# Kernel tuning notes

Measured on AMD Instinct MI355X. Metric: run time of the kernel, lower is better.

## Reference

```python
import jax, jax.numpy as jnp
import numpy as np

NUM_HEADS = 12
DIM = 768
NV = 4  # number of views
EPS = 1e-6


def _ln(x, g, b):
    m = x.mean(-1, keepdims=True)
    v = ((x - m) ** 2).mean(-1, keepdims=True)
    return (x - m) / jnp.sqrt(v + EPS) * g + b


def setup_inputs() -> dict:
    key = jax.random.key(0)
    ks = jax.random.split(key, 10)
    B, N, C, H = 4, 256, DIM, NUM_HEADS
    Hid = 4 * C
    s = 0.02
    return {
        'X': jax.random.normal(ks[0], (B * NV, N, C), jnp.float32),
        'norm1_g': jnp.ones((C,), jnp.float32),
        'norm1_b': jnp.zeros((C,), jnp.float32),
        'qkv_w': jax.random.normal(ks[1], (NV, 3 * C, C), jnp.float32) * s,
        'proj_w': jax.random.normal(ks[2], (NV, C, C), jnp.float32) * s,
        'proj_b': jnp.zeros((NV, C), jnp.float32),
        'norm2_g': jnp.ones((NV, C), jnp.float32),
        'norm2_b': jnp.zeros((NV, C), jnp.float32),
        'fc1_w': jax.random.normal(ks[3], (NV, Hid, C), jnp.float32) * s,
        'fc1_b': jnp.zeros((NV, Hid), jnp.float32),
        'fc2_w': jax.random.normal(ks[4], (NV, C, Hid), jnp.float32) * s,
        'fc2_b': jnp.zeros((NV, C), jnp.float32),
        'query': jax.random.normal(ks[5], (1, 1, C), jnp.float32),
        'mha_in_w': jax.random.normal(ks[6], (NV, 3 * C, C), jnp.float32) * s,
        'mha_in_b': jnp.zeros((NV, 3 * C), jnp.float32),
        'mha_out_w': jax.random.normal(ks[7], (NV, C, C), jnp.float32) * s,
        'mha_out_b': jnp.zeros((NV, C), jnp.float32),
    }


def reference(X, norm1_g, norm1_b, qkv_w, proj_w, proj_b, norm2_g, norm2_b,
              fc1_w, fc1_b, fc2_w, fc2_b, query, mha_in_w, mha_in_b,
              mha_out_w, mha_out_b):
    B4, N, C = X.shape
    B = B4 // NV
    H = NUM_HEADS
    hd = C // H
    scale = hd ** -0.5

    Xv = X.reshape(B, NV, N, C)
    Xn = _ln(Xv, norm1_g, norm1_b)

    # ---- FusionAttention: 4x4 pairwise cross attention between views ----
    qkv = jnp.einsum('bvnc,vdc->vbnd', Xn, qkv_w)              # [V,B,N,3C]
    qkv = qkv.reshape(NV, B, N, 3, H, hd).transpose(3, 0, 1, 4, 2, 5)  # [3,V,B,H,N,hd]
    q, k, v = qkv[0], qkv[1], qkv[2]
    scores = jnp.einsum('ibhnd,jbhmd->ijbhnm', q, k) * scale   # [V,V,B,H,N,N]
    attn = jax.nn.softmax(scores, axis=-1)
    ctx = jnp.einsum('ijbhnm,jbhmd->ijbhnd', attn, v)
    ctx = ctx.transpose(0, 1, 2, 4, 3, 5).reshape(NV, NV, B, N, C)
    # proj_i is affine, so mean over j of proj(x_j) == proj(mean_j x_j)
    ctx_mean = ctx.mean(axis=1)                                # [V,B,N,C]
    xa = jnp.einsum('vbnc,voc->vbno', ctx_mean, proj_w) + proj_b[:, None, None, :]

    x = xa * 2.0
    h = _ln(x, norm2_g[:, None, None, :], norm2_b[:, None, None, :])
    h1 = jax.nn.gelu(jnp.einsum('vbnc,vhc->vbnh', h, fc1_w) + fc1_b[:, None, None, :],
                     approximate=False)
    h2 = jnp.einsum('vbnh,vch->vbnc', h1, fc2_w) + fc2_b[:, None, None, :]
    x = x + h2                                                  # [V,B,N,C]

    # ---- CrossAttentionWithLearnableQuery (query identical for all T,B) ----
    wq, wk, wv = jnp.split(mha_in_w, 3, axis=1)                 # each [V,C,C]
    bq, bk, bv = jnp.split(mha_in_b, 3, axis=1)                 # each [V,C]
    q0 = query.reshape(C)
    qh = (jnp.einsum('c,vdc->vd', q0, wq) + bq).reshape(NV, H, hd)
    kh = (jnp.einsum('vbnc,vdc->vbnd', x, wk) + bk[:, None, None, :]).reshape(NV, B, N, H, hd)
    vh = (jnp.einsum('vbnc,vdc->vbnd', x, wv) + bv[:, None, None, :]).reshape(NV, B, N, H, hd)
    s2 = jnp.einsum('vhd,vbnhd->vbhn', qh, kh) * scale
    a2 = jax.nn.softmax(s2, axis=-1)
    c2 = jnp.einsum('vbhn,vbnhd->vbhd', a2, vh).reshape(NV, B, C)
    o = jnp.einsum('vbc,voc->vbo', c2, mha_out_w) + mha_out_b[:, None, :]  # [V,B,C]
    o = o.transpose(1, 0, 2).reshape(B, NV * C)                 # concat views
    # every query position produces identical output -> broadcast over T=N
    return jnp.broadcast_to(o[:, None, :], (B, N, NV * C))
```

## Files before the change

kernel.cpp:

```cpp
#include <hip/hip_runtime.h>
#include <math.h>

#define NVIEW 4
#define BATCH 4
#define NSEQ  256
#define CDIM  768
#define HEADS 12
#define HD    64

typedef __attribute__((ext_vector_type(8))) short   short8;
typedef __attribute__((ext_vector_type(8))) unsigned short ushort8;
typedef __attribute__((ext_vector_type(4))) float   float4v;

typedef const __attribute__((address_space(1))) void gas_t;
typedef       __attribute__((address_space(3))) void las_t;

__device__ __forceinline__ unsigned short f2b(float x)
{
    union { float f; unsigned u; } c; c.f = x;
    unsigned r = (c.u + 0x7FFFu + ((c.u >> 16) & 1u)) >> 16;
    return (unsigned short)r;
}

__global__ void conv_bf16(const float* __restrict__ src, unsigned short* __restrict__ dst, int n)
{
    int idx = (blockIdx.x * 256 + threadIdx.x) * 8;
    if (idx >= n) return;
    float4 a = *(const float4*)(src + idx);
    float4 b = *(const float4*)(src + idx + 4);
    ushort8 o;
    o[0] = f2b(a.x); o[1] = f2b(a.y); o[2] = f2b(a.z); o[3] = f2b(a.w);
    o[4] = f2b(b.x); o[5] = f2b(b.y); o[6] = f2b(b.z); o[7] = f2b(b.w);
    *(ushort8*)(dst + idx) = o;
}

__device__ __forceinline__ void block_ln_row_b(const float* __restrict__ xrow,
                                               const float* __restrict__ g,
                                               const float* __restrict__ b,
                                               unsigned short* __restrict__ orow)
{
    const int t = threadIdx.x;
    float x0 = xrow[t], x1 = xrow[t + 256], x2 = xrow[t + 512];
    float s  = x0 + x1 + x2;
    float s2 = x0 * x0 + x1 * x1 + x2 * x2;
    #pragma unroll
    for (int off = 32; off > 0; off >>= 1) {
        s  += __shfl_down(s, off);
        s2 += __shfl_down(s2, off);
    }
    __shared__ float w1[4], w2[4];
    if ((t & 63) == 0) { w1[t >> 6] = s; w2[t >> 6] = s2; }
    __syncthreads();
    float S  = w1[0] + w1[1] + w1[2] + w1[3];
    float S2 = w2[0] + w2[1] + w2[2] + w2[3];
    float mean = S * (1.0f / 768.0f);
    float var  = S2 * (1.0f / 768.0f) - mean * mean;
    float inv  = rsqrtf(var + 1e-6f);
    orow[t]       = f2b((x0 - mean) * inv * g[t]       + b[t]);
    orow[t + 256] = f2b((x1 - mean) * inv * g[t + 256] + b[t + 256]);
    orow[t + 512] = f2b((x2 - mean) * inv * g[t + 512] + b[t + 512]);
}

__global__ void ln1_kernel(const float* __restrict__ X, const float* __restrict__ g,
                           const float* __restrict__ b, unsigned short* __restrict__ Xn)
{
    int rid = blockIdx.x;
    int n  = rid & 255;
    int bv = rid >> 8;
    int bb = bv >> 2, v = bv & 3;
    const float* xrow = X + (long)rid * CDIM;
    unsigned short* orow = Xn + ((long)(v * 4 + bb) * 256 + n) * CDIM;
    block_ln_row_b(xrow, g, b, orow);
}

__global__ void ln2_kernel(const float* __restrict__ Xin, const float* __restrict__ g,
                           const float* __restrict__ b, unsigned short* __restrict__ Out)
{
    int rid = blockIdx.x;
    int v = rid >> 10;
    const float* xrow = Xin + (long)rid * CDIM;
    block_ln_row_b(xrow, g + v * CDIM, b + v * CDIM, Out + (long)rid * CDIM);
}

template <int EPI, int TM, typename OT>
__launch_bounds__(256, 2)
__global__ void gemm_bf16(const unsigned short* __restrict__ A,
                          const unsigned short* __restrict__ W,
                          const float* __restrict__ bias, const float* __restrict__ resid,
                          OT* __restrict__ out, int M, int N, int K,
                          long wStride, long wOff, int bStride, int bOff)
{
    const int v = blockIdx.z;
    const unsigned short* Av = A + (long)v * M * K;
    const unsigned short* Wv = W + v * wStride + wOff;

    __shared__ unsigned short As[TM * 64];
    __shared__ unsigned short Bs[128 * 64];

    const int tid  = threadIdx.x;
    const int lane = tid & 63;
    const int wave = tid >> 6;
    const int l15  = lane & 15;
    const int quad = lane >> 4;
    const int row0 = blockIdx.y * TM, col0 = blockIdx.x * 128;

    constexpr int MI = 4;
    constexpr int NI = (TM == 128) ? 4 : 2;
    const int mw = (TM == 128) ? (wave & 1) * 64 : 0;
    const int nw = (TM == 128) ? (wave >> 1) * 64 : wave * 32;

    float4v acc[MI][NI];
    #pragma unroll
    for (int i = 0; i < MI; ++i)
        #pragma unroll
        for (int j = 0; j < NI; ++j)
            acc[i][j] = (float4v){0.f, 0.f, 0.f, 0.f};

    const int lr8 = lane >> 3;
    const int p8  = lane & 7;

    for (int k0 = 0; k0 < K; k0 += 64) {
        __syncthreads();
        #pragma unroll
        for (int g = 0; g < TM / 32; ++g) {
            int G = wave * (TM / 32) + g;
            int r = G * 8 + lr8;
            int c = p8 ^ (r & 7);
            const unsigned short* sa = Av + (long)(row0 + r) * K + k0 + c * 8;
            __builtin_amdgcn_global_load_lds((gas_t*)sa, (las_t*)&As[G * 512], 16, 0, 0);
        }
        #pragma unroll
        for (int g = 0; g < 4; ++g) {
            int G = wave * 4 + g;
            int r = G * 8 + lr8;
            int c = p8 ^ (r & 7);
            const unsigned short* sw = Wv + (long)(col0 + r) * K + k0 + c * 8;
            __builtin_amdgcn_global_load_lds((gas_t*)sw, (las_t*)&Bs[G * 512], 16, 0, 0);
        }
        __syncthreads();

        #pragma unroll
        for (int ks = 0; ks < 2; ++ks) {
            short8 af[MI], bfr[NI];
            #pragma unroll
            for (int mi = 0; mi < MI; ++mi) {
                int m = mw + mi * 16 + l15;
                int p = (ks * 4 + quad) ^ (m & 7);
                af[mi] = *(const short8*)&As[m * 64 + p * 8];
            }
            #pragma unroll
            for (int ni = 0; ni < NI; ++ni) {
                int n = nw + ni * 16 + l15;
                int p = (ks * 4 + quad) ^ (n & 7);
                bfr[ni] = *(const short8*)&Bs[n * 64 + p * 8];
            }
            #pragma unroll
            for (int mi = 0; mi < MI; ++mi)
                #pragma unroll
                for (int ni = 0; ni < NI; ++ni)
                    acc[mi][ni] = __builtin_amdgcn_mfma_f32_16x16x32_bf16(af[mi], bfr[ni], acc[mi][ni], 0, 0, 0);
        }
    }

    #pragma unroll
    for (int mi = 0; mi < MI; ++mi) {
        #pragma unroll
        for (int ni = 0; ni < NI; ++ni) {
            int rowb = row0 + mw + mi * 16 + quad * 4;
            int col  = col0 + nw + ni * 16 + l15;
            float bval = 0.f;
            if (EPI >= 1) bval = bias[v * bStride + bOff + col];
            #pragma unroll
            for (int r = 0; r < 4; ++r) {
                float x = acc[mi][ni][r] + bval;
                long off = (long)v * M * N + (long)(rowb + r) * N + col;
                if constexpr (EPI == 2) {
                    x = 0.5f * x * (1.0f + erff(x * 0.70710678118654752f));
                } else if constexpr (EPI == 3) {
                    x += resid[off];
                } else if constexpr (EPI == 4) {
                    x *= 2.0f;
                }
                if constexpr (sizeof(OT) == 2) ((unsigned short*)out)[off] = f2b(x);
                else                           ((float*)out)[off] = x;
            }
        }
    }
}

__launch_bounds__(256, 2)
__global__ void fusion_attn_mfma(const unsigned short* __restrict__ QKV,
                                 unsigned short* __restrict__ ctx)
{
    const int qt = blockIdx.x;
    const int b  = blockIdx.y / HEADS;
    const int h  = blockIdx.y % HEADS;
    const int i  = blockIdx.z;
    const int tid  = threadIdx.x;
    const int lane = tid & 63;
    const int wave = tid >> 6;
    const int l15  = lane & 15;
    const int quad = lane >> 4;

    __shared__ unsigned short Qs[64 * 72];
    __shared__ unsigned short Ks[128 * 64];
    __shared__ unsigned short Ps[64 * 136];
    __shared__ unsigned short Vt[64 * 136];

    {
        int r = tid >> 2, p16 = (tid & 3) * 16;
        const unsigned short* src = QKV + ((long)((i * 4 + b) * 256 + qt * 64 + r)) * 2304 + h * 64 + p16;
        *(ushort8*)(&Qs[r * 72 + p16])     = *(const ushort8*)(src);
        *(ushort8*)(&Qs[r * 72 + p16 + 8]) = *(const ushort8*)(src + 8);
    }

    float4v acc_o[4];
    #pragma unroll
    for (int e = 0; e < 4; ++e) acc_o[e] = (float4v){0.f, 0.f, 0.f, 0.f};

    for (int j = 0; j < 4; ++j) {
        const unsigned short* Kb = QKV + ((long)((j * 4 + b) * 256)) * 2304 + 768 + h * 64;
        const unsigned short* Vb = Kb + 768;

        float4v sacc[16];
        #pragma unroll
        for (int t = 0; t < 16; ++t) sacc[t] = (float4v){0.f, 0.f, 0.f, 0.f};

        for (int half = 0; half < 2; ++half) {
            __syncthreads();
            #pragma unroll
            for (int g = 0; g < 4; ++g) {
                int R = wave * 32 + g * 8;
                int r = R + (lane >> 3);
                int p = lane & 7;
                int c = (p - (r & 7)) & 7;
                const unsigned short* src = Kb + (long)(half * 128 + r) * 2304 + c * 8;
                __builtin_amdgcn_global_load_lds((gas_t*)src, (las_t*)&Ks[R * 64], 16, 0, 0);
            }
            __syncthreads();
            #pragma unroll
            for (int ks = 0; ks < 2; ++ks) {
                int lcq = ks * 4 + quad;
                short8 qf = *(const short8*)&Qs[(wave * 16 + l15) * 72 + lcq * 8];
                #pragma unroll
                for (int nn = 0; nn < 8; ++nn) {
                    int n = nn * 16 + l15;
                    int p = (lcq + (n & 7)) & 7;
                    short8 kf = *(const short8*)&Ks[n * 64 + p * 8];
                    sacc[half * 8 + nn] =
                        __builtin_amdgcn_mfma_f32_16x16x32_bf16(qf, kf, sacc[half * 8 + nn], 0, 0, 0);
                }
            }
        }

        float rmax[4] = {-1e30f, -1e30f, -1e30f, -1e30f};
        #pragma unroll
        for (int t = 0; t < 16; ++t)
            #pragma unroll
            for (int r = 0; r < 4; ++r)
                rmax[r] = fmaxf(rmax[r], sacc[t][r] * 0.125f);
        #pragma unroll
        for (int off = 1; off < 16; off <<= 1)
            #pragma unroll
            for (int r = 0; r < 4; ++r)
                rmax[r] = fmaxf(rmax[r], __shfl_xor(rmax[r], off));
        float rsum[4] = {0.f, 0.f, 0.f, 0.f};
        #pragma unroll
        for (int t = 0; t < 16; ++t)
            #pragma unroll
            for (int r = 0; r < 4; ++r) {
                float e = __expf(sacc[t][r] * 0.125f - rmax[r]);
                sacc[t][r] = e;
                rsum[r] += e;
            }
        #pragma unroll
        for (int off = 1; off < 16; off <<= 1)
            #pragma unroll
            for (int r = 0; r < 4; ++r)
                rsum[r] += __shfl_xor(rsum[r], off);
        float invl[4];
        #pragma unroll
        for (int r = 0; r < 4; ++r) invl[r] = 1.0f / rsum[r];

        float4v pv[4];
        #pragma unroll
        for (int e = 0; e < 4; ++e) pv[e] = (float4v){0.f, 0.f, 0.f, 0.f};

        for (int half = 0; half < 2; ++half) {
            __syncthreads();
            #pragma unroll
            for (int nn = 0; nn < 8; ++nn)
                #pragma unroll
                for (int r = 0; r < 4; ++r)
                    Ps[(wave * 16 + quad * 4 + r) * 136 + nn * 16 + l15] = f2b(sacc[half * 8 + nn][r]);
            {
                int n = tid & 127;
                int c0 = (tid >> 7) * 4;
                #pragma unroll
                for (int cc = 0; cc < 4; ++cc) {
                    int c = c0 + cc;
                    ushort8 vv = *(const ushort8*)(Vb + (long)(half * 128 + n) * 2304 + c * 8);
                    #pragma unroll
                    for (int jj = 0; jj < 8; ++jj)
                        Vt[(c * 8 + jj) * 136 + n] = vv[jj];
                }
            }
            __syncthreads();
            #pragma unroll
            for (int ks = 0; ks < 4; ++ks) {
                int lc = ks * 4 + quad;
                short8 pf = *(const short8*)&Ps[(wave * 16 + l15) * 136 + lc * 8];
                #pragma unroll
                for (int et = 0; et < 4; ++et) {
                    short8 vf = *(const short8*)&Vt[(et * 16 + l15) * 136 + lc * 8];
                    pv[et] = __builtin_amdgcn_mfma_f32_16x16x32_bf16(pf, vf, pv[et], 0, 0, 0);
                }
            }
        }
        #pragma unroll
        for (int et = 0; et < 4; ++et)
            #pragma unroll
            for (int r = 0; r < 4; ++r)
                acc_o[et][r] += pv[et][r] * invl[r];
    }

    #pragma unroll
    for (int et = 0; et < 4; ++et)
        #pragma unroll
        for (int r = 0; r < 4; ++r) {
            int row = (i * 4 + b) * 256 + qt * 64 + wave * 16 + quad * 4 + r;
            int col = h * 64 + et * 16 + l15;
            ctx[(long)row * 768 + col] = f2b(acc_o[et][r] * 0.25f);
        }
}

__launch_bounds__(256, 4)
__global__ void qh_kernel(const float* __restrict__ query, const float* __restrict__ Win,
                          const float* __restrict__ Bin, float* __restrict__ QH)
{
    const int bi   = blockIdx.x;
    const int v    = bi / 192;
    const int dblk = bi - v * 192;
    const int t    = threadIdx.x;
    const int wave = t >> 6;
    const int lane = t & 63;
    const int d    = dblk * 4 + wave;

    __shared__ float qs[768];
    for (int idx = t; idx < 768; idx += 256) qs[idx] = query[idx];
    __syncthreads();

    const float* w = Win + ((long)v * 2304 + d) * 768;
    float acc = 0.f;
    #pragma unroll
    for (int k = 0; k < 3; ++k) {
        int c = k * 256 + lane * 4;
        float4 w4 = *(const float4*)(w + c);
        float4 q4 = *(const float4*)&qs[c];
        acc += w4.x * q4.x + w4.y * q4.y + w4.z * q4.z + w4.w * q4.w;
    }
    #pragma unroll
    for (int off = 32; off > 0; off >>= 1) acc += __shfl_down(acc, off);
    if (lane == 0)
        QH[v * 768 + d] = acc + Bin[(long)v * 2304 + d];
}

__launch_bounds__(256, 2)
__global__ void cross_attn(const float* __restrict__ KVH, const float* __restrict__ QH,
                           float* __restrict__ C2)
{
    const int h = blockIdx.x, b = blockIdx.y, v = blockIdx.z;
    const int t = threadIdx.x;
    __shared__ float qv[64];
    __shared__ float p[256];
    __shared__ float part[4][64];
    __shared__ float wred[4], wred2[4];

    if (t < 64) qv[t] = QH[(v * 12 + h) * 64 + t];
    __syncthreads();

    const float* krow = KVH + ((long)((v * 4 + b) * 256 + t)) * 1536 + h * 64;
    float s = 0.f;
    #pragma unroll
    for (int e = 0; e < 64; e += 4) {
        float4 k4 = *(const float4*)(krow + e);
        s += qv[e] * k4.x + qv[e + 1] * k4.y + qv[e + 2] * k4.z + qv[e + 3] * k4.w;
    }
    s *= 0.125f;
    float m4 = s;
    #pragma unroll
    for (int off = 32; off > 0; off >>= 1) m4 = fmaxf(m4, __shfl_down(m4, off));
    if ((t & 63) == 0) wred[t >> 6] = m4;
    __syncthreads();
    float rmax = fmaxf(fmaxf(wred[0], wred[1]), fmaxf(wred[2], wred[3]));
    float ev = __expf(s - rmax);
    p[t] = ev;
    float s4 = ev;
    #pragma unroll
    for (int off = 32; off > 0; off >>= 1) s4 += __shfl_down(s4, off);
    if ((t & 63) == 0) wred2[t >> 6] = s4;
    __syncthreads();
    float inv = 1.0f / (wred2[0] + wred2[1] + wred2[2] + wred2[3]);

    const int e = t & 63, ch = t >> 6;
    const float* vbase = KVH + ((long)((v * 4 + b) * 256)) * 1536 + 768 + h * 64 + e;
    float accv = 0.f;
    for (int m = ch * 64; m < ch * 64 + 64; ++m)
        accv += p[m] * vbase[(long)m * 1536];
    part[ch][e] = accv;
    __syncthreads();
    if (t < 64)
        C2[(v * 4 + b) * 768 + h * 64 + t] =
            (part[0][t] + part[1][t] + part[2][t] + part[3][t]) * inv;
}

__launch_bounds__(256, 4)
__global__ void out_matvec(const float* __restrict__ C2, const float* __restrict__ Wout,
                           const float* __restrict__ Bout, float* __restrict__ obc)
{
    const int bi   = blockIdx.x;
    const int v    = bi / 192;
    const int dblk = bi - v * 192;
    const int t    = threadIdx.x;
    const int wave = t >> 6;
    const int lane = t & 63;
    const int d    = dblk * 4 + wave;

    __shared__ float c2s[3072];
    #pragma unroll
    for (int idx = 0; idx < 3072; idx += 256) c2s[idx + t] = C2[v * 3072 + idx + t];
    __syncthreads();

    const float* w = Wout + ((long)v * 768 + d) * 768;
    float acc0 = 0.f, acc1 = 0.f, acc2 = 0.f, acc3 = 0.f;
    #pragma unroll
    for (int k = 0; k < 3; ++k) {
        int c = k * 256 + lane * 4;
        float4 w4 = *(const float4*)(w + c);
        float4 a0 = *(const float4*)&c2s[c];
        float4 a1 = *(const float4*)&c2s[768 + c];
        float4 a2 = *(const float4*)&c2s[1536 + c];
        float4 a3 = *(const float4*)&c2s[2304 + c];
        acc0 += w4.x * a0.x + w4.y * a0.y + w4.z * a0.z + w4.w * a0.w;
        acc1 += w4.x * a1.x + w4.y * a1.y + w4.z * a1.z + w4.w * a1.w;
        acc2 += w4.x * a2.x + w4.y * a2.y + w4.z * a2.z + w4.w * a2.w;
        acc3 += w4.x * a3.x + w4.y * a3.y + w4.z * a3.z + w4.w * a3.w;
    }
    #pragma unroll
    for (int off = 32; off > 0; off >>= 1) {
        acc0 += __shfl_down(acc0, off);
        acc1 += __shfl_down(acc1, off);
        acc2 += __shfl_down(acc2, off);
        acc3 += __shfl_down(acc3, off);
    }
    if (lane == 0) {
        float bb = Bout[v * 768 + d];
        obc[0 * 3072 + v * 768 + d] = acc0 + bb;
        obc[1 * 3072 + v * 768 + d] = acc1 + bb;
        obc[2 * 3072 + v * 768 + d] = acc2 + bb;
        obc[3 * 3072 + v * 768 + d] = acc3 + bb;
    }
}

__launch_bounds__(256, 4)
__global__ void out_bcast(const float* __restrict__ obc, float* __restrict__ out)
{
    const int b  = blockIdx.x >> 6;
    const int n0 = (blockIdx.x & 63) * 4;
    const int t  = threadIdx.x;
    const float4* src = (const float4*)(obc + (long)b * 3072);
    float4 v0 = src[t], v1 = src[t + 256], v2 = src[t + 512];
    float4* dst = (float4*)(out + ((long)(b * 256 + n0)) * 3072);
    #pragma unroll
    for (int r = 0; r < 4; ++r) {
        dst[r * 768 + t]       = v0;
        dst[r * 768 + t + 256] = v1;
        dst[r * 768 + t + 512] = v2;
    }
}

extern "C" void kernel_launch(void* const* d_in, const int* in_sizes, int n_in,
                              void* d_out, int out_size, void* d_ws, size_t ws_size,
                              hipStream_t stream)
{
    const float* X        = (const float*)d_in[0];
    const float* n1g      = (const float*)d_in[1];
    const float* n1b      = (const float*)d_in[2];
    const float* qkv_w    = (const float*)d_in[3];
    const float* proj_w   = (const float*)d_in[4];
    const float* proj_b   = (const float*)d_in[5];
    const float* n2g      = (const float*)d_in[6];
    const float* n2b      = (const float*)d_in[7];
    const float* fc1_w    = (const float*)d_in[8];
    const float* fc1_b    = (const float*)d_in[9];
    const float* fc2_w    = (const float*)d_in[10];
    const float* fc2_b    = (const float*)d_in[11];
    const float* query    = (const float*)d_in[12];
    const float* mha_in_w = (const float*)d_in[13];
    const float* mha_in_b = (const float*)d_in[14];
    const float* mha_out_w= (const float*)d_in[15];
    const float* mha_out_b= (const float*)d_in[16];
    float* out = (float*)d_out;

    char* wsb = (char*)d_ws;
    unsigned short* wbuf = (unsigned short*)wsb;
    unsigned short* rgA  = (unsigned short*)(wsb + 18874368);
    char*           rgB  = wsb + 25165824;
    float*          xbuf = (float*)(wsb + 50331648);
    float*          qh   = (float*)(wsb + 62914560);
    float*          c2   = (float*)(wsb + 62926848);
    float*          obc  = (float*)(wsb + 62976000);

    unsigned short* QKV = (unsigned short*)rgB;
    unsigned short* H1  = (unsigned short*)rgB;
    float*          KVH = (float*)rgB;

    conv_bf16<<<3456, 256, 0, stream>>>(qkv_w, wbuf, 7077888);
    ln1_kernel<<<4096, 256, 0, stream>>>(X, n1g, n1b, rgA);
    gemm_bf16<0, 128, unsigned short><<<dim3(18, 8, 4), 256, 0, stream>>>(
        rgA, wbuf, nullptr, nullptr, QKV, 1024, 2304, 768, 2304L * 768, 0, 0, 0);
    fusion_attn_mfma<<<dim3(4, 48, 4), 256, 0, stream>>>(QKV, rgA);
    conv_bf16<<<1152, 256, 0, stream>>>(proj_w, wbuf, 2359296);
    gemm_bf16<4, 64, float><<<dim3(6, 16, 4), 256, 0, stream>>>(
        rgA, wbuf, proj_b, nullptr, xbuf, 1024, 768, 768, 768L * 768, 0, 768, 0);
    ln2_kernel<<<4096, 256, 0, stream>>>(xbuf, n2g, n2b, rgA);
    conv_bf16<<<4608, 256, 0, stream>>>(fc1_w, wbuf, 9437184);
    gemm_bf16<2, 128, unsigned short><<<dim3(24, 8, 4), 256, 0, stream>>>(
        rgA, wbuf, fc1_b, nullptr, H1, 1024, 3072, 768, 3072L * 768, 0, 3072, 0);
    conv_bf16<<<4608, 256, 0, stream>>>(fc2_w, wbuf, 9437184);
    gemm_bf16<3, 64, unsigned short><<<dim3(6, 16, 4), 256, 0, stream>>>(
        H1, wbuf, fc2_b, xbuf, rgA, 1024, 768, 3072, 768L * 3072, 0, 768, 0);
    conv_bf16<<<3456, 256, 0, stream>>>(mha_in_w, wbuf, 7077888);
    gemm_bf16<1, 64, float><<<dim3(12, 16, 4), 256, 0, stream>>>(
        rgA, wbuf, mha_in_b, nullptr, KVH, 1024, 1536, 768, 2304L * 768, 768L * 768, 2304, 768);
    qh_kernel<<<768, 256, 0, stream>>>(query, mha_in_w, mha_in_b, qh);
    cross_attn<<<dim3(12, 4, 4), 256, 0, stream>>>(KVH, qh, c2);
    out_matvec<<<768, 256, 0, stream>>>(c2, mha_out_w, mha_out_b, obc);
    out_bcast<<<256, 256, 0, stream>>>(obc, out);
}
```

Baseline: 436.2 us.

## Restructure fusion attention: transposed MFMA, shared K/V buffer, prefetched V, packed stores

Rewrites the fusion attention kernel so the QK and PV MFMAs use swapped operands, which puts each query row in one lane and reduces the softmax to two cross-lane shuffles. K and the transposed V now share one LDS buffer, shrinking LDS so occupancy can rise to 3 blocks per CU. V loads are issued into registers ahead of time so they overlap with the QK MFMAs, with explicit waitcnt, barriers and setprio. P, V-transpose and output writes become packed 64-bit stores. The hand-placed waitcnt and barriers are more fragile, and the extra register pressure may clash with the higher occupancy bound.

Measured after the change: 425.0 us. 1.03x faster.

```diff
diff --git a/kernel.cpp b/kernel.cpp
--- a/kernel.cpp
+++ b/kernel.cpp
@@ -20,6 +20,11 @@
     union { float f; unsigned u; } c; c.f = x;
     unsigned r = (c.u + 0x7FFFu + ((c.u >> 16) & 1u)) >> 16;
     return (unsigned short)r;
+}
+
+__device__ __forceinline__ unsigned pack2b(float a, float b)
+{
+    return (unsigned)f2b(a) | ((unsigned)f2b(b) << 16);
 }
 
 __global__ void conv_bf16(const float* __restrict__ src, unsigned short* __restrict__ dst, int n)
@@ -188,7 +193,7 @@
     }
 }
 
-__launch_bounds__(256, 2)
+__launch_bounds__(256, 3)
 __global__ void fusion_attn_mfma(const unsigned short* __restrict__ QKV,
                                  unsigned short* __restrict__ ctx)
 {
@@ -203,9 +208,8 @@
     const int quad = lane >> 4;
 
     __shared__ unsigned short Qs[64 * 72];
-    __shared__ unsigned short Ks[128 * 64];
+    __shared__ unsigned short KVu[64 * 136];
     __shared__ unsigned short Ps[64 * 136];
-    __shared__ unsigned short Vt[64 * 136];
 
     {
         int r = tid >> 2, p16 = (tid & 3) * 16;
@@ -214,6 +218,9 @@
         *(ushort8*)(&Qs[r * 72 + p16 + 8]) = *(const ushort8*)(src + 8);
     }
 
+    const int kg = tid & 31;
+    const int dc = tid >> 5;
+
     float4v acc_o[4];
     #pragma unroll
     for (int e = 0; e < 4; ++e) acc_o[e] = (float4v){0.f, 0.f, 0.f, 0.f};
@@ -226,112 +233,171 @@
         #pragma unroll
         for (int t = 0; t < 16; ++t) sacc[t] = (float4v){0.f, 0.f, 0.f, 0.f};
 
-        for (int half = 0; half < 2; ++half) {
-            __syncthreads();
-            #pragma unroll
-            for (int g = 0; g < 4; ++g) {
-                int R = wave * 32 + g * 8;
-                int r = R + (lane >> 3);
-                int p = lane & 7;
-                int c = (p - (r & 7)) & 7;
-                const unsigned short* src = Kb + (long)(half * 128 + r) * 2304 + c * 8;
-                __builtin_amdgcn_global_load_lds((gas_t*)src, (las_t*)&Ks[R * 64], 16, 0, 0);
-            }
-            __syncthreads();
-            #pragma unroll
-            for (int ks = 0; ks < 2; ++ks) {
-                int lcq = ks * 4 + quad;
-                short8 qf = *(const short8*)&Qs[(wave * 16 + l15) * 72 + lcq * 8];
-                #pragma unroll
-                for (int nn = 0; nn < 8; ++nn) {
-                    int n = nn * 16 + l15;
-                    int p = (lcq + (n & 7)) & 7;
-                    short8 kf = *(const short8*)&Ks[n * 64 + p * 8];
-                    sacc[half * 8 + nn] =
-                        __builtin_amdgcn_mfma_f32_16x16x32_bf16(qf, kf, sacc[half * 8 + nn], 0, 0, 0);
-                }
-            }
-        }
-
-        float rmax[4] = {-1e30f, -1e30f, -1e30f, -1e30f};
+        ushort8 vv0[4], vv1[4];
+
+        __syncthreads();
+        #pragma unroll
+        for (int g = 0; g < 4; ++g) {
+            int R = wave * 32 + g * 8;
+            int r = R + (lane >> 3);
+            int p = lane & 7;
+            int c = (p - (r & 7)) & 7;
+            const unsigned short* src = Kb + (long)(r) * 2304 + c * 8;
+            __builtin_amdgcn_global_load_lds((gas_t*)src, (las_t*)&KVu[R * 64], 16, 0, 0);
+        }
+        __syncthreads();
+        __builtin_amdgcn_s_setprio(1);
+        #pragma unroll
+        for (int ks = 0; ks < 2; ++ks) {
+            int lcq = ks * 4 + quad;
+            short8 qf = *(const short8*)&Qs[(wave * 16 + l15) * 72 + lcq * 8];
+            #pragma unroll
+            for (int nn = 0; nn < 8; ++nn) {
+                int n = nn * 16 + l15;
+                int p = (lcq + (n & 7)) & 7;
+                short8 kf = *(const short8*)&KVu[n * 64 + p * 8];
+                sacc[nn] = __builtin_amdgcn_mfma_f32_16x16x32_bf16(kf, qf, sacc[nn], 0, 0, 0);
+            }
+        }
+        __builtin_amdgcn_s_setprio(0);
+
+        __syncthreads();
+        #pragma unroll
+        for (int g = 0; g < 4; ++g) {
+            int R = wave * 32 + g * 8;
+            int r = R + (lane >> 3);
+            int p = lane & 7;
+            int c = (p - (r & 7)) & 7;
+            const unsigned short* src = Kb + (long)(128 + r) * 2304 + c * 8;
+            __builtin_amdgcn_global_load_lds((gas_t*)src, (las_t*)&KVu[R * 64], 16, 0, 0);
+        }
+        __builtin_amdgcn_sched_barrier(0);
+        #pragma unroll
+        for (int q = 0; q < 4; ++q)
+            vv0[q] = *(const ushort8*)(Vb + (long)(kg * 4 + q) * 2304 + dc * 8);
+        asm volatile("s_waitcnt vmcnt(4) lgkmcnt(0)" ::: "memory");
+        __builtin_amdgcn_s_barrier();
+        __builtin_amdgcn_sched_barrier(0);
+        __builtin_amdgcn_s_setprio(1);
+        #pragma unroll
+        for (int ks = 0; ks < 2; ++ks) {
+            int lcq = ks * 4 + quad;
+            short8 qf = *(const short8*)&Qs[(wave * 16 + l15) * 72 + lcq * 8];
+            #pragma unroll
+            for (int nn = 0; nn < 8; ++nn) {
+                int n = nn * 16 + l15;
+                int p = (lcq + (n & 7)) & 7;
+                short8 kf = *(const short8*)&KVu[n * 64 + p * 8];
+                sacc[8 + nn] = __builtin_amdgcn_mfma_f32_16x16x32_bf16(kf, qf, sacc[8 + nn], 0, 0, 0);
+            }
+        }
+        __builtin_amdgcn_s_setprio(0);
+
+        float m = -1e30f;
         #pragma unroll
         for (int t = 0; t < 16; ++t)
             #pragma unroll
+            for (int r = 0; r < 4; ++r) {
+                sacc[t][r] *= 0.125f;
+                m = fmaxf(m, sacc[t][r]);
+            }
+        m = fmaxf(m, __shfl_xor(m, 16));
+        m = fmaxf(m, __shfl_xor(m, 32));
+        float lsum = 0.f;
+        #pragma unroll
+        for (int t = 0; t < 16; ++t)
+            #pragma unroll
+            for (int r = 0; r < 4; ++r) {
+                float e = __expf(sacc[t][r] - m);
+                sacc[t][r] = e;
+                lsum += e;
+            }
+        lsum += __shfl_xor(lsum, 16);
+        lsum += __shfl_xor(lsum, 32);
+        float invl = 1.0f / lsum;
+
+        float4v pv[4];
+        #pragma unroll
+        for (int e = 0; e < 4; ++e) pv[e] = (float4v){0.f, 0.f, 0.f, 0.f};
+
+        __syncthreads();
+        #pragma unroll
+        for (int nn = 0; nn < 8; ++nn) {
+            unsigned lo = pack2b(sacc[nn][0], sacc[nn][1]);
+            unsigned hi = pack2b(sacc[nn][2], sacc[nn][3]);
+            *(unsigned long long*)&Ps[(wave * 16 + l15) * 136 + nn * 16 + quad * 4] =
+                ((unsigned long long)hi << 32) | lo;
+        }
+        #pragma unroll
+        for (int jj = 0; jj < 8; ++jj) {
+            unsigned lo = (unsigned)vv0[0][jj] | ((unsigned)vv0[1][jj] << 16);
+            unsigned hi = (unsigned)vv0[2][jj] | ((unsigned)vv0[3][jj] << 16);
+            *(unsigned long long*)&KVu[(dc * 8 + jj) * 136 + kg * 4] =
+                ((unsigned long long)hi << 32) | lo;
+        }
+        #pragma unroll
+        for (int q = 0; q < 4; ++q)
+            vv1[q] = *(const ushort8*)(Vb + (long)(128 + kg * 4 + q) * 2304 + dc * 8);
+        asm volatile("s_waitcnt lgkmcnt(0)" ::: "memory");
+        __builtin_amdgcn_s_barrier();
+        __builtin_amdgcn_sched_barrier(0);
+        __builtin_amdgcn_s_setprio(1);
+        #pragma unroll
+        for (int ks = 0; ks < 4; ++ks) {
+            int lc = ks * 4 + quad;
+            short8 pf = *(const short8*)&Ps[(wave * 16 + l15) * 136 + lc * 8];
+            #pragma unroll
+            for (int et = 0; et < 4; ++et) {
+                short8 vf = *(const short8*)&KVu[(et * 16 + l15) * 136 + lc * 8];
+                pv[et] = __builtin_amdgcn_mfma_f32_16x16x32_bf16(vf, pf, pv[et], 0, 0, 0);
+            }
+        }
+        __builtin_amdgcn_s_setprio(0);
+
+        __syncthreads();
+        #pragma unroll
+        for (int nn = 0; nn < 8; ++nn) {
+            unsigned lo = pack2b(sacc[8 + nn][0], sacc[8 + nn][1]);
+            unsigned hi = pack2b(sacc[8 + nn][2], sacc[8 + nn][3]);
+            *(unsigned long long*)&Ps[(wave * 16 + l15) * 136 + nn * 16 + quad * 4] =
+                ((unsigned long long)hi << 32) | lo;
+        }
+        #pragma unroll
+        for (int jj = 0; jj < 8; ++jj) {
+            unsigned lo = (unsigned)vv1[0][jj] | ((unsigned)vv1[1][jj] << 16);
+            unsigned hi = (unsigned)vv1[2][jj] | ((unsigned)vv1[3][jj] << 16);
+            *(unsigned long long*)&KVu[(dc * 8 + jj) * 136 + kg * 4] =
+                ((unsigned long long)hi << 32) | lo;
+        }
+        __syncthreads();
+        __builtin_amdgcn_s_setprio(1);
+        #pragma unroll
+        for (int ks = 0; ks < 4; ++ks) {
+            int lc = ks * 4 + quad;
+            short8 pf = *(const short8*)&Ps[(wave * 16 + l15) * 136 + lc * 8];
+            #pragma unroll
+            for (int et = 0; et < 4; ++et) {
+                short8 vf = *(const short8*)&KVu[(et * 16 + l15) * 136 + lc * 8];
+                pv[et] = __builtin_amdgcn_mfma_f32_16x16x32_bf16(vf, pf, pv[et], 0, 0, 0);
+            }
+        }
+        __builtin_amdgcn_s_setprio(0);
+
+        #pragma unroll
+        for (int et = 0; et < 4; ++et)
+            #pragma unroll
             for (int r = 0; r < 4; ++r)
-                rmax[r] = fmaxf(rmax[r], sacc[t][r] * 0.125f);
-        #pragma unroll
-        for (int off = 1; off < 16; off <<= 1)
-            #pragma unroll
-            for (int r = 0; r < 4; ++r)
-                rmax[r] = fmaxf(rmax[r], __shfl_xor(rmax[r], off));
-        float rsum[4] = {0.f, 0.f, 0.f, 0.f};
-        #pragma unroll
-        for (int t = 0; t < 16; ++t)
-            #pragma unroll
-            for (int r = 0; r < 4; ++r) {
-                float e = __expf(sacc[t][r] * 0.125f - rmax[r]);
-                sacc[t][r] = e;
-                rsum[r] += e;
-            }
-        #pragma unroll
-        for (int off = 1; off < 16; off <<= 1)
-            #pragma unroll
-            for (int r = 0; r < 4; ++r)
-                rsum[r] += __shfl_xor(rsum[r], off);
-        float invl[4];
-        #pragma unroll
-        for (int r = 0; r < 4; ++r) invl[r] = 1.0f / rsum[r];
-
-        float4v pv[4];
-        #pragma unroll
-        for (int e = 0; e < 4; ++e) pv[e] = (float4v){0.f, 0.f, 0.f, 0.f};
-
-        for (int half = 0; half < 2; ++half) {
-            __syncthreads();
-            #pragma unroll
-            for (int nn = 0; nn < 8; ++nn)
-                #pragma unroll
-                for (int r = 0; r < 4; ++r)
-                    Ps[(wave * 16 + quad * 4 + r) * 136 + nn * 16 + l15] = f2b(sacc[half * 8 + nn][r]);
-            {
-                int n = tid & 127;
-                int c0 = (tid >> 7) * 4;
-                #pragma unroll
-                for (int cc = 0; cc < 4; ++cc) {
-                    int c = c0 + cc;
-                    ushort8 vv = *(const ushort8*)(Vb + (long)(half * 128 + n) * 2304 + c * 8);
-                    #pragma unroll
-                    for (int jj = 0; jj < 8; ++jj)
-                        Vt[(c * 8 + jj) * 136 + n] = vv[jj];
-                }
-            }
-            __syncthreads();
-            #pragma unroll
-            for (int ks = 0; ks < 4; ++ks) {
-                int lc = ks * 4 + quad;
-                short8 pf = *(const short8*)&Ps[(wave * 16 + l15) * 136 + lc * 8];
-                #pragma unroll
-                for (int et = 0; et < 4; ++et) {
-                    short8 vf = *(const short8*)&Vt[(et * 16 + l15) * 136 + lc * 8];
-                    pv[et] = __builtin_amdgcn_mfma_f32_16x16x32_bf16(pf, vf, pv[et], 0, 0, 0);
-                }
-            }
-        }
-        #pragma unroll
-        for (int et = 0; et < 4; ++et)
-            #pragma unroll
-            for (int r = 0; r < 4; ++r)
-                acc_o[et][r] += pv[et][r] * invl[r];
-    }
-
-    #pragma unroll
-    for (int et = 0; et < 4; ++et)
-        #pragma unroll
-        for (int r = 0; r < 4; ++r) {
-            int row = (i * 4 + b) * 256 + qt * 64 + wave * 16 + quad * 4 + r;
-            int col = h * 64 + et * 16 + l15;
-            ctx[(long)row * 768 + col] = f2b(acc_o[et][r] * 0.25f);
-        }
+                acc_o[et][r] += pv[et][r] * invl;
+    }
+
+    #pragma unroll
+    for (int et = 0; et < 4; ++et) {
+        unsigned lo = pack2b(acc_o[et][0] * 0.25f, acc_o[et][1] * 0.25f);
+        unsigned hi = pack2b(acc_o[et][2] * 0.25f, acc_o[et][3] * 0.25f);
+        long row = (long)((i * 4 + b) * 256 + qt * 64 + wave * 16 + l15);
+        int  col = h * 64 + et * 16 + quad * 4;
+        *(unsigned long long*)&ctx[row * 768 + col] = ((unsigned long long)hi << 32) | lo;
+    }
 }
 
 __launch_bounds__(256, 4)
```
